# Kernel tuning notes

Measured on AMD Instinct MI355X. Metric: run time of the kernel, lower is better.

Reference implementation:

```python
import jax, jax.numpy as jnp
import numpy as np

B, L, D = 4, 1024, 1024
H = 16
HD = D // H
SCALE = HD ** -0.5
LOCAL_WINDOW = 32
HALF = LOCAL_WINDOW // 2
TEMP = 1.0
PATTERN_TEMP = 1.0
THRESHOLD = 0.1
SPARSITY_RATIO = 0.3
# k for learned sparse topk (eval mode, static given L)
EFF = min(SPARSITY_RATIO, 1.0 - 10.0 / L)
K_TOP = max(1, min(L, int(L * (1.0 - EFF))))


def setup_inputs() -> dict:
    key = jax.random.key(0)
    ks = jax.random.split(key, 16)
    def xavier(k, shape, gain=1.0):
        fan_in, fan_out = shape[1], shape[0]
        a = gain * np.sqrt(6.0 / (fan_in + fan_out))
        return jax.random.uniform(k, shape, jnp.float32, -a, a)
    return {
        'x': jax.random.normal(ks[0], (B, L, D), jnp.float32),
        'w_qkv': xavier(ks[1], (3 * D, D), gain=1.0 / np.sqrt(2.0)),
        'w_proj': xavier(ks[2], (D, D)),
        'b_proj': jnp.zeros((D,), jnp.float32),
        'ps_w1': xavier(ks[3], (D, D), gain=0.5),
        'ps_b1': jnp.zeros((D,), jnp.float32),
        'ln_g': jnp.ones((D,), jnp.float32),
        'ln_b': jnp.zeros((D,), jnp.float32),
        'ps_w2': xavier(ks[4], (D // 2, D), gain=0.5),
        'ps_b2': jnp.zeros((D // 2,), jnp.float32),
        'ps_w3': xavier(ks[5], (3, D // 2), gain=0.5),
        'ps_b3': jnp.zeros((3,), jnp.float32),
        'pattern_bias': jnp.array([0.05, 0.0, -0.05], jnp.float32),
        'sparse_w': jax.random.normal(ks[6], (H, 1, 1), jnp.float32) * 0.1 + 1.0,
        'sparse_b': jnp.zeros((H, 1, 1), jnp.float32),
    }


def _forward(x, w_qkv, w_proj, b_proj, ps_w1, ps_b1, ln_g, ln_b,
             ps_w2, ps_b2, ps_w3, ps_b3, pattern_bias, sparse_w, sparse_b):
    qkv = (x @ w_qkv.T).reshape(B, L, 3, H, HD)
    qkv = jnp.transpose(qkv, (2, 0, 3, 1, 4))  # [3,B,H,L,HD]
    q, k, v = qkv[0], qkv[1], qkv[2]
    scores = jnp.einsum('bhid,bhjd->bhij', q, k) * SCALE  # [B,H,L,L]

    # pattern selector on pooled features
    pooled = (jnp.mean(x, axis=1) + jnp.max(x, axis=1)) / 2.0  # [B,D]
    h = pooled @ ps_w1.T + ps_b1
    mu = jnp.mean(h, axis=-1, keepdims=True)
    var = jnp.mean((h - mu) ** 2, axis=-1, keepdims=True)
    h = (h - mu) / jnp.sqrt(var + 1e-5) * ln_g + ln_b
    h = jax.nn.gelu(h, approximate=False)
    h = jax.nn.gelu(h @ ps_w2.T + ps_b2, approximate=False)
    logits = h @ ps_w3.T + ps_b3 + pattern_bias  # [B,3]
    pw = jax.nn.softmax(logits / PATTERN_TEMP, axis=-1)  # [B,3]

    # learned sparse mask via per-head affine + topk scatter
    s2 = scores * jnp.abs(sparse_w)[None] + sparse_b[None]  # [B,H,L,L]
    _, topk_idx = jax.lax.top_k(s2, K_TOP)  # [B,H,L,K]
    bi = jnp.arange(B)[:, None, None, None]
    hi = jnp.arange(H)[None, :, None, None]
    li = jnp.arange(L)[None, None, :, None]
    sparse_mask = jnp.zeros_like(scores).at[bi, hi, li, topk_idx].set(1.0)

    # local sliding-window mask |i-j| <= HALF
    i = jnp.arange(L)
    local = (jnp.abs(i[:, None] - i[None, :]) <= HALF).astype(jnp.float32)  # [L,L]

    combined = (pw[:, 0, None, None, None] * local[None, None]
                + pw[:, 1, None, None, None]
                + pw[:, 2, None, None, None] * sparse_mask)
    binary = combined > THRESHOLD
    scores = jnp.where(binary, scores, -jnp.inf)

    # fallback: rows fully masked attend only to themselves (score 0)
    all_masked = ~jnp.any(binary, axis=-1)  # [B,H,L]
    eye = jnp.eye(L, dtype=bool)
    scores = jnp.where(all_masked[..., None] & eye[None, None], 0.0, scores)

    attn = jax.nn.softmax(scores / TEMP, axis=-1)
    out = jnp.einsum('bhij,bhjd->bhid', attn, v)  # [B,H,L,HD]
    out = jnp.transpose(out, (0, 2, 1, 3)).reshape(B, L, D)
    return out @ w_proj.T + b_proj


def reference(x, w_qkv, w_proj, b_proj, ps_w1, ps_b1, ln_g, ln_b,
              ps_w2, ps_b2, ps_w3, ps_b3, pattern_bias, sparse_w, sparse_b):
    return _forward(x, w_qkv, w_proj, b_proj, ps_w1, ps_b1, ln_g, ln_b,
                    ps_w2, ps_b2, ps_w3, ps_b3, pattern_bias, sparse_w, sparse_b)
```

## Files before the change

kernel.cpp:

```cpp
#include <hip/hip_runtime.h>
#include <math.h>

#define KTOP_ 716
#define SCALE_ 0.125f
#define QSCALE_ 0.1803368801111731f
#define LN2_ 0.6931471805599453f

typedef float f4v __attribute__((ext_vector_type(4)));
typedef short s8v __attribute__((ext_vector_type(8)));
typedef __bf16 bf8v __attribute__((ext_vector_type(8)));

static __device__ inline unsigned short f2bf(float f) {
  unsigned u = __float_as_uint(f);
  u += 0x7fffu + ((u >> 16) & 1u);
  return (unsigned short)(u >> 16);
}
static __device__ inline unsigned short f2bfn(float f) {
  union { __bf16 b; unsigned short u; } cv;
  cv.b = (__bf16)f;
  return cv.u;
}
static __device__ inline float bf2f(unsigned short h) {
  return __uint_as_float((unsigned)h << 16);
}
static __device__ inline f4v mfma16(s8v a, s8v b, f4v c) {
  union { s8v s; bf8v b; } ua, ub;
  ua.s = a; ub.s = b;
  return __builtin_amdgcn_mfma_f32_16x16x32_bf16(ua.b, ub.b, c, 0, 0, 0);
}
static __device__ inline void gload16(const unsigned short* g, unsigned short* lbase) {
  __builtin_amdgcn_global_load_lds(
      (const __attribute__((address_space(1))) unsigned int*)g,
      (__attribute__((address_space(3))) unsigned int*)lbase, 16, 0, 0);
}

__global__ __launch_bounds__(256) void pool1(const float* __restrict__ x,
                                             float* __restrict__ psum,
                                             float* __restrict__ pmax,
                                             unsigned short* __restrict__ xs) {
  int bid = blockIdx.x;
  int b = bid >> 6, sl = bid & 63;
  int t = threadIdx.x;
  float s[4] = {0.f, 0.f, 0.f, 0.f};
  float m[4] = {-INFINITY, -INFINITY, -INFINITY, -INFINITY};
  const float* xb = x + ((size_t)b << 20) + (size_t)sl * 16 * 1024;
  unsigned short* xo = xs + ((size_t)(b * 1024 + sl * 16)) * 1024;
  for (int l = 0; l < 16; ++l) {
    #pragma unroll
    for (int dg = 0; dg < 4; ++dg) {
      float v = xb[l * 1024 + dg * 256 + t];
      s[dg] += v;
      m[dg] = fmaxf(m[dg], v);
      xo[(size_t)l * 1024 + dg * 256 + t] = f2bfn(v);
    }
  }
  #pragma unroll
  for (int dg = 0; dg < 4; ++dg) {
    psum[(size_t)bid * 1024 + dg * 256 + t] = s[dg];
    pmax[(size_t)bid * 1024 + dg * 256 + t] = m[dg];
  }
}

__global__ __launch_bounds__(256) void ps_gemv1(const float* __restrict__ psum,
                                                const float* __restrict__ pmax,
                                                const float* __restrict__ w1,
                                                const float* __restrict__ b1,
                                                float* __restrict__ h1) {
  __shared__ float pool_s[1024];
  int bid = blockIdx.x;
  int b = bid >> 4, og = bid & 15;
  int t = threadIdx.x;
  #pragma unroll
  for (int i = 0; i < 4; ++i) {
    int d = t + 256 * i;
    float s = 0.f, m = -INFINITY;
    #pragma unroll 8
    for (int sl = 0; sl < 64; ++sl) {
      s += psum[((size_t)b * 64 + sl) * 1024 + d];
      m = fmaxf(m, pmax[((size_t)b * 64 + sl) * 1024 + d]);
    }
    pool_s[d] = (s * (1.0f / 1024.0f) + m) * 0.5f;
  }
  __syncthreads();
  int ol = t >> 2, ks = t & 3;
  int o = og * 64 + ol;
  const float4* wr = (const float4*)(w1 + (size_t)o * 1024 + ks * 256);
  const float4* pp = (const float4*)(&pool_s[ks * 256]);
  float acc = 0.f;
  #pragma unroll 8
  for (int j = 0; j < 64; ++j) {
    float4 a = wr[j], p = pp[j];
    acc += a.x * p.x + a.y * p.y + a.z * p.z + a.w * p.w;
  }
  acc += __shfl_xor(acc, 1, 64);
  acc += __shfl_xor(acc, 2, 64);
  if (ks == 0) h1[b * 1024 + o] = acc + b1[o];
}

__global__ __launch_bounds__(256) void ps_gemv2(const float* __restrict__ h1,
                                                const float* __restrict__ lng,
                                                const float* __restrict__ lnb,
                                                const float* __restrict__ w2,
                                                const float* __restrict__ b2,
                                                float* __restrict__ h2) {
  __shared__ float hs[1024];
  __shared__ float red[256];
  int bid = blockIdx.x;
  int b = bid >> 3, og = bid & 7;
  int t = threadIdx.x;
  const float* hb = h1 + b * 1024;
  float v0[4];
  float ls = 0.f;
  #pragma unroll
  for (int i = 0; i < 4; ++i) { v0[i] = hb[t + 256 * i]; ls += v0[i]; }
  red[t] = ls; __syncthreads();
  for (int s = 128; s > 0; s >>= 1) { if (t < s) red[t] += red[t + s]; __syncthreads(); }
  float mean = red[0] * (1.0f / 1024.0f);
  __syncthreads();
  float lq = 0.f;
  #pragma unroll
  for (int i = 0; i < 4; ++i) { float dv = v0[i] - mean; lq += dv * dv; }
  red[t] = lq; __syncthreads();
  for (int s = 128; s > 0; s >>= 1) { if (t < s) red[t] += red[t + s]; __syncthreads(); }
  float rstd = 1.0f / sqrtf(red[0] * (1.0f / 1024.0f) + 1e-5f);
  #pragma unroll
  for (int i = 0; i < 4; ++i) {
    float v = (v0[i] - mean) * rstd * lng[t + 256 * i] + lnb[t + 256 * i];
    hs[t + 256 * i] = 0.5f * v * (1.0f + erff(v * 0.70710678118654752f));
  }
  __syncthreads();
  int ol = t >> 2, ks = t & 3;
  int o = og * 64 + ol;
  const float4* wr = (const float4*)(w2 + (size_t)o * 1024 + ks * 256);
  const float4* pp = (const float4*)(&hs[ks * 256]);
  float acc = 0.f;
  #pragma unroll 8
  for (int j = 0; j < 64; ++j) {
    float4 a = wr[j], p = pp[j];
    acc += a.x * p.x + a.y * p.y + a.z * p.z + a.w * p.w;
  }
  acc += __shfl_xor(acc, 1, 64);
  acc += __shfl_xor(acc, 2, 64);
  if (ks == 0) {
    float v = acc + b2[o];
    h2[b * 512 + o] = 0.5f * v * (1.0f + erff(v * 0.70710678118654752f));
  }
}

__global__ __launch_bounds__(256) void ps_logits(const float* __restrict__ h2,
                                                 const float* __restrict__ w3,
                                                 const float* __restrict__ b3,
                                                 const float* __restrict__ pb,
                                                 int* __restrict__ meta) {
  __shared__ float red[256];
  int b = blockIdx.x, t = threadIdx.x;
  float lgv[3];
  for (int c = 0; c < 3; ++c) {
    float p = 0.f;
    for (int i = t; i < 512; i += 256) p += h2[b * 512 + i] * w3[c * 512 + i];
    red[t] = p; __syncthreads();
    for (int s = 128; s > 0; s >>= 1) { if (t < s) red[t] += red[t + s]; __syncthreads(); }
    lgv[c] = red[0] + b3[c] + pb[c];
    __syncthreads();
  }
  if (t == 0) {
    float mx = fmaxf(lgv[0], fmaxf(lgv[1], lgv[2]));
    float e0 = __expf(lgv[0] - mx), e1 = __expf(lgv[1] - mx), e2 = __expf(lgv[2] - mx);
    float inv = 1.0f / (e0 + e1 + e2);
    float p0 = e0 * inv, p1 = e1 * inv, p2 = e2 * inv;
    float c00 = p1;
    float c10 = p0 + p1;
    float c01 = p1 + p2;
    float c11 = (p0 + p1) + p2;
    int t00 = c00 > 0.1f, t10 = c10 > 0.1f, t01 = c01 > 0.1f, t11 = c11 > 0.1f;
    meta[b * 8 + 0] = t00;
    meta[b * 8 + 1] = t10;
    meta[b * 8 + 2] = t01;
    meta[b * 8 + 3] = t11;
    meta[b * 8 + 4] = (t00 != t01) || (t10 != t11);
  }
}

__global__ __launch_bounds__(256) void prep_w(const float* __restrict__ w_qkv,
                                              const float* __restrict__ w_proj,
                                              unsigned short* __restrict__ wqs,
                                              unsigned short* __restrict__ wps) {
  int i = blockIdx.x * 256 + threadIdx.x;
  const float* src;
  unsigned short* dst;
  int idx;
  if (i < 786432) { src = w_qkv; dst = wqs; idx = i; }
  else            { src = w_proj; dst = wps; idx = i - 786432; }
  float4 v = ((const float4*)src)[idx];
  ushort4 o;
  o.x = f2bfn(v.x); o.y = f2bfn(v.y); o.z = f2bfn(v.z); o.w = f2bfn(v.w);
  *(ushort4*)(dst + (size_t)idx * 4) = o;
}

template <int MODE, int TM>
__global__ __launch_bounds__(256) void gemm_sp(
    const unsigned short* __restrict__ A, const unsigned short* __restrict__ B,
    const float* __restrict__ bias,
    unsigned short* __restrict__ qxo, unsigned short* __restrict__ kxo,
    unsigned short* __restrict__ vxo,
    float* __restrict__ out, int Nb) {
  constexpr int MFR = TM / 32;
  __shared__ unsigned short Asm[2][TM * 64];
  __shared__ unsigned short Bsm[2][128 * 64];

  int bid = blockIdx.x;
  int bm, bn;
  if (MODE == 0) {
    int xcd = bid & 7, idx = bid >> 3;
    int rb = (xcd >> 1) * 8, cb = (xcd & 1) * 12;
    int r, c;
    if (idx < 64) { r = idx & 7; c = idx >> 3; }
    else          { int j = idx - 64; r = j & 7; c = 8 + (j >> 3); }
    bm = rb + r; bn = cb + c;
  } else {
    int cpx = gridDim.x >> 3;
    int g = (bid & 7) * cpx + (bid >> 3);
    bm = g / Nb; bn = g % Nb;
  }
  size_t row0 = (size_t)bm * TM, col0 = (size_t)bn * 128;

  int tid = threadIdx.x, lane = tid & 63, wv = tid >> 6;
  int wm = (wv >> 1) * (MFR * 16), wn = (wv & 1) << 6;
  int rowg = lane >> 4, colc = lane & 15;

  f4v acc[MFR][4];
  #pragma unroll
  for (int mf = 0; mf < MFR; ++mf)
    #pragma unroll
    for (int nf = 0; nf < 4; ++nf) acc[mf][nf] = (f4v){0.f, 0.f, 0.f, 0.f};

  const unsigned short* Abase = A + row0 * 1024;
  const unsigned short* Bbase = B + col0 * 1024;

  auto STAGE = [&](int kb, int buf) {
    #pragma unroll
    for (int p = 0; p < TM / 32; ++p) {
      int idx = p * 256 + tid;
      int row = idx >> 3;
      int sc = (idx & 7) ^ (row & 7);
      gload16(Abase + (size_t)row * 1024 + kb + sc * 8,
              &Asm[buf][(size_t)(p * 256 + wv * 64) * 8]);
    }
    #pragma unroll
    for (int p = 0; p < 4; ++p) {
      int idx = p * 256 + tid;
      int row = idx >> 3;
      int sc = (idx & 7) ^ (row & 7);
      gload16(Bbase + (size_t)row * 1024 + kb + sc * 8,
              &Bsm[buf][(size_t)(p * 256 + wv * 64) * 8]);
    }
  };

  STAGE(0, 0);
  __syncthreads();
  int cur = 0;

  for (int kb = 0; kb < 1024; kb += 64) {
    if (kb + 64 < 1024) STAGE(kb + 64, cur ^ 1);
    #pragma unroll
    for (int ks = 0; ks < 2; ++ks) {
      s8v af[MFR], bf_[4];
      #pragma unroll
      for (int mf = 0; mf < MFR; ++mf) {
        int row = wm + mf * 16 + colc;
        int kby = (ks * 64 + rowg * 16) ^ ((row & 7) << 4);
        af[mf] = *(const s8v*)((const char*)&Asm[cur][0] + row * 128 + kby);
      }
      #pragma unroll
      for (int nf = 0; nf < 4; ++nf) {
        int row = wn + nf * 16 + colc;
        int kby = (ks * 64 + rowg * 16) ^ ((row & 7) << 4);
        bf_[nf] = *(const s8v*)((const char*)&Bsm[cur][0] + row * 128 + kby);
      }
      #pragma unroll
      for (int mf = 0; mf < MFR; ++mf)
        #pragma unroll
        for (int nf = 0; nf < 4; ++nf)
          acc[mf][nf] = mfma16(af[mf], bf_[nf], acc[mf][nf]);
    }
    __syncthreads();
    cur ^= 1;
  }

  if (MODE == 0) {
    int c = (int)(col0 >> 10);
    #pragma unroll
    for (int mf = 0; mf < MFR; ++mf) {
      int m0 = (int)row0 + wm + mf * 16 + rowg * 4;
      int bb = m0 >> 10, l0 = m0 & 1023;
      #pragma unroll
      for (int nf = 0; nf < 4; ++nf) {
        int n = (int)col0 + wn + nf * 16 + colc;
        int hh = (n >> 6) & 15, hd = n & 63;
        int bhl = bb * 16 + hh;
        if (c == 2) {
          ushort4 h4;
          h4.x = f2bfn(acc[mf][nf][0]);
          h4.y = f2bfn(acc[mf][nf][1]);
          h4.z = f2bfn(acc[mf][nf][2]);
          h4.w = f2bfn(acc[mf][nf][3]);
          *(ushort4*)(vxo + ((size_t)bhl * 64 + hd) * 1024 + l0) = h4;
        } else {
          unsigned short* dst = ((c == 0) ? qxo : kxo) +
                                ((size_t)bhl * 1024 + l0) * 64 + hd;
          float sc_ = (c == 0) ? QSCALE_ : 1.0f;
          #pragma unroll
          for (int r = 0; r < 4; ++r)
            dst[(size_t)r * 64] = f2bfn(acc[mf][nf][r] * sc_);
        }
      }
    }
  } else {
    #pragma unroll
    for (int mf = 0; mf < MFR; ++mf) {
      #pragma unroll
      for (int r = 0; r < 4; ++r) {
        int m = (int)row0 + wm + mf * 16 + rowg * 4 + r;
        #pragma unroll
        for (int nf = 0; nf < 4; ++nf) {
          int n = (int)col0 + wn + nf * 16 + colc;
          out[(size_t)m * 1024 + n] = acc[mf][nf][r] + bias[n];
        }
      }
    }
  }
}

__global__ __launch_bounds__(256) void attn_flash(
    const unsigned short* __restrict__ qx, const unsigned short* __restrict__ kx,
    const unsigned short* __restrict__ vx, const int* __restrict__ meta,
    unsigned short* __restrict__ ao) {
  int n = blockIdx.x;
  int bh = ((n & 7) << 3) | (n >> 7);
  int qt = (n >> 3) & 15;
  int b = bh >> 4, h = bh & 15;
  const int* mb = meta + b * 8;
  if (mb[4]) return;
  int t00 = mb[0], t10 = mb[1];

  int tid = threadIdx.x, lane = tid & 63, wv = tid >> 6;
  int g = lane >> 4, colc = lane & 15;
  int q0 = qt * 64 + wv * 16;

  if (!t10) {
    #pragma unroll
    for (int it = 0; it < 4; ++it) {
      int idx = tid + it * 256;
      int r = idx >> 4, dc = (idx & 15) * 4;
      ushort4 o;
      unsigned short* op = (unsigned short*)&o;
      #pragma unroll
      for (int j = 0; j < 4; ++j)
        op[j] = vx[((size_t)bh * 64 + dc + j) * 1024 + qt * 64 + r];
      *(ushort4*)(ao + ((size_t)b * 1024 + qt * 64 + r) * 1024 + h * 64 + dc) = o;
    }
    return;
  }
  bool local_only = !t00;

  __shared__ __align__(16) unsigned short Ksm[2][64 * 64];
  __shared__ __align__(16) unsigned short Vsm[2][64 * 64];
  __shared__ __align__(16) unsigned short px[4][16][64];

  const unsigned short* qb = qx + ((size_t)bh * 1024 + q0 + colc) * 64 + g * 8;
  s8v Q0 = *(const s8v*)(qb);
  s8v Q1 = *(const s8v*)(qb + 32);

  f4v O[4];
  #pragma unroll
  for (int df = 0; df < 4; ++df) O[df] = (f4v){0.f, 0.f, 0.f, 0.f};
  float m = -1e30f, lsum = 0.f;

  const unsigned short* kxb = kx + ((size_t)bh << 10) * 64;
  const unsigned short* vxb = vx + ((size_t)bh << 16);
  int bq0 = qt * 64;

  int jb_lo = 0, jb_hi = 15;
  if (local_only) {
    int lo = (bq0 - 16) >> 6, hi = (bq0 + 79) >> 6;
    jb_lo = lo < 0 ? 0 : lo;
    jb_hi = hi > 15 ? 15 : hi;
  }

  auto STAGE = [&](int jb2, int buf) {
    int jc = jb2 << 6;
    #pragma unroll
    for (int p = 0; p < 2; ++p) {
      int cidx = p * 256 + tid;
      int row = cidx >> 3;
      int sc = (cidx & 7) ^ (row & 7);
      gload16(kxb + (size_t)(jc + row) * 64 + sc * 8,
              &Ksm[buf][(size_t)(p * 256 + wv * 64) * 8]);
      gload16(vxb + (size_t)row * 1024 + jc + sc * 8,
              &Vsm[buf][(size_t)(p * 256 + wv * 64) * 8]);
    }
  };

  STAGE(jb_lo, 0);
  __syncthreads();
  int cur = 0;
  int swk = (colc & 7) << 4;
  int sx = (colc & 7) << 1;

  for (int jb = jb_lo; jb <= jb_hi; ++jb) {
    if (jb < jb_hi) STAGE(jb + 1, cur ^ 1);

    int jc0 = jb << 6;
    bool wact = !(local_only && (jc0 + 63 < q0 - 16 || jc0 > q0 + 31));
    if (wact) {
      f4v s[4];
      #pragma unroll
      for (int jf = 0; jf < 4; ++jf) {
        const char* kp = (const char*)&Ksm[cur][0] + (jf * 16 + colc) * 128;
        s8v K0 = *(const s8v*)(kp + ((g * 16) ^ swk));
        s8v K1 = *(const s8v*)(kp + ((64 + g * 16) ^ swk));
        f4v acc = (f4v){0.f, 0.f, 0.f, 0.f};
        acc = mfma16(K0, Q0, acc);
        acc = mfma16(K1, Q1, acc);
        s[jf] = acc;
      }

      if (local_only) {
        int i = q0 + colc;
        #pragma unroll
        for (int jf = 0; jf < 4; ++jf)
          #pragma unroll
          for (int r = 0; r < 4; ++r) {
            int j = jc0 + jf * 16 + 4 * g + r;
            int dj = i - j;
            if (dj > 16 || dj < -16) s[jf][r] = -1e30f;
          }
      }

      float cm = fmaxf(
          fmaxf(fmaxf(fmaxf(s[0][0], s[0][1]), fmaxf(s[0][2], s[0][3])),
                fmaxf(fmaxf(s[1][0], s[1][1]), fmaxf(s[1][2], s[1][3]))),
          fmaxf(fmaxf(fmaxf(s[2][0], s[2][1]), fmaxf(s[2][2], s[2][3])),
                fmaxf(fmaxf(s[3][0], s[3][1]), fmaxf(s[3][2], s[3][3]))));
      cm = fmaxf(cm, __shfl_xor(cm, 16, 64));
      cm = fmaxf(cm, __shfl_xor(cm, 32, 64));

      if (__any(cm > m + 8.0f)) {
        float mn = fmaxf(m, cm);
        float fac = __builtin_amdgcn_exp2f(m - mn);
        m = mn;
        lsum *= fac;
        float fo[4];
        #pragma unroll
        for (int r = 0; r < 4; ++r)
          fo[r] = __shfl(fac, (lane & 48) + g * 4 + r, 64);
        #pragma unroll
        for (int df = 0; df < 4; ++df)
          #pragma unroll
          for (int r = 0; r < 4; ++r) O[df][r] *= fo[r];
      }

      float psum = 0.f;
      #pragma unroll
      for (int jf = 0; jf < 4; ++jf) {
        float p0 = __builtin_amdgcn_exp2f(s[jf][0] - m);
        float p1 = __builtin_amdgcn_exp2f(s[jf][1] - m);
        float p2 = __builtin_amdgcn_exp2f(s[jf][2] - m);
        float p3 = __builtin_amdgcn_exp2f(s[jf][3] - m);
        psum += (p0 + p1) + (p2 + p3);
        ushort4 pk;
        pk.x = f2bfn(p0); pk.y = f2bfn(p1); pk.z = f2bfn(p2); pk.w = f2bfn(p3);
        *(ushort4*)&px[wv][colc][4 * ((jf * 4 + g) ^ sx)] = pk;
      }
      psum += __shfl_xor(psum, 16, 64);
      psum += __shfl_xor(psum, 32, 64);
      lsum += psum;

      s8v Pf[2];
      #pragma unroll
      for (int ks = 0; ks < 2; ++ks)
        Pf[ks] = *(const s8v*)&px[wv][colc][4 * ((ks * 8 + 2 * g) ^ sx)];
      #pragma unroll
      for (int df = 0; df < 4; ++df) {
        const char* vp = (const char*)&Vsm[cur][0] + (df * 16 + colc) * 128;
        #pragma unroll
        for (int ks = 0; ks < 2; ++ks) {
          s8v Vf = *(const s8v*)(vp + ((ks * 64 + g * 16) ^ swk));
          O[df] = mfma16(Pf[ks], Vf, O[df]);
        }
      }
    }
    __syncthreads();
    cur ^= 1;
  }

  float linv[4];
  #pragma unroll
  for (int r = 0; r < 4; ++r)
    linv[r] = 1.0f / __shfl(lsum, (lane & 48) + g * 4 + r, 64);
  #pragma unroll
  for (int df = 0; df < 4; ++df) {
    #pragma unroll
    for (int r = 0; r < 4; ++r) {
      int i = q0 + g * 4 + r;
      ao[((size_t)b * 1024 + i) * 1024 + h * 64 + df * 16 + colc] =
          f2bfn(O[df][r] * linv[r]);
    }
  }
}

__global__ __launch_bounds__(256) void attn_sparse(
    const unsigned short* __restrict__ qx, const unsigned short* __restrict__ kx,
    const unsigned short* __restrict__ vx, const int* __restrict__ meta,
    unsigned short* __restrict__ ao) {
  __shared__ float S[32][1028];
  __shared__ float qs[32][68];
  __shared__ float kc[64][68];
  __shared__ float rowsum_s[32];

  int tid = threadIdx.x;
  int lane = tid & 63;
  int wv = tid >> 6;
  int id = blockIdx.x;
  int rt = id & 31;
  int h = (id >> 5) & 15;
  int b = id >> 9;
  int bh = b * 16 + h;
  int row0 = rt * 32;

  const int* mb = meta + b * 8;
  int t00 = mb[0], t10 = mb[1], t01 = mb[2], t11 = mb[3], needs = mb[4];
  if (!needs) return;

  #pragma unroll
  for (int i = 0; i < 8; ++i) {
    int idx = tid + 256 * i;
    int r = idx >> 6, d = idx & 63;
    qs[r][d] = bf2f(qx[((size_t)bh * 1024 + row0 + r) * 64 + d]);
  }

  int lr = lane >> 4, lc = lane & 15;
  int r_a = wv * 8 + lr * 2;
  int r_b = r_a + 1;

  for (int cb = 0; cb < 16; ++cb) {
    __syncthreads();
    #pragma unroll
    for (int i = 0; i < 2; ++i) {
      int idx = tid + 256 * i;
      int cc = idx >> 3, d0 = (idx & 7) * 8;
      union { s8v v; unsigned short u[8]; } kv8;
      kv8.v = *(const s8v*)(kx + ((size_t)bh * 1024 + cb * 64 + cc) * 64 + d0);
      #pragma unroll
      for (int j = 0; j < 8; ++j) kc[cc][d0 + j] = bf2f(kv8.u[j]);
    }
    __syncthreads();

    float acc0[4] = {0.f, 0.f, 0.f, 0.f};
    float acc1[4] = {0.f, 0.f, 0.f, 0.f};
    for (int dq = 0; dq < 64; dq += 4) {
      float4 qa = *(const float4*)&qs[r_a][dq];
      float4 qb = *(const float4*)&qs[r_b][dq];
      #pragma unroll
      for (int cj = 0; cj < 4; ++cj) {
        float4 kv = *(const float4*)&kc[lc + 16 * cj][dq];
        acc0[cj] += qa.x * kv.x + qa.y * kv.y + qa.z * kv.z + qa.w * kv.w;
        acc1[cj] += qb.x * kv.x + qb.y * kv.y + qb.z * kv.z + qb.w * kv.w;
      }
    }
    #pragma unroll
    for (int cj = 0; cj < 4; ++cj) {
      S[r_a][cb * 64 + lc + 16 * cj] = acc0[cj] * LN2_;
      S[r_b][cb * 64 + lc + 16 * cj] = acc1[cj] * LN2_;
    }
  }

  for (int rr = 0; rr < 8; ++rr) {
    int r = wv * 8 + rr;
    int grow = row0 + r;
    float sv[16];
    unsigned kv[16];
    #pragma unroll
    for (int i2 = 0; i2 < 16; ++i2) {
      float s = S[r][lane + 64 * i2];
      sv[i2] = s;
      unsigned u = __float_as_uint(s);
      kv[i2] = (u & 0x80000000u) ? ~u : (u | 0x80000000u);
    }
    unsigned T = 0u;
    for (int bit = 31; bit >= 0; --bit) {
      unsigned cand = T | (1u << bit);
      int cnt = 0;
      #pragma unroll
      for (int i2 = 0; i2 < 16; ++i2) cnt += (kv[i2] >= cand) ? 1 : 0;
      for (int off = 32; off; off >>= 1) cnt += __shfl_xor(cnt, off, 64);
      if (cnt >= KTOP_) T = cand;
    }
    float mx = -INFINITY;
    int kept = 0;
    unsigned kmask = 0;
    #pragma unroll
    for (int i2 = 0; i2 < 16; ++i2) {
      int j = lane + 64 * i2;
      int sp = (kv[i2] >= T) ? 1 : 0;
      int dj = grow - j;
      int lo = (dj <= 16 && dj >= -16) ? 1 : 0;
      int keep = sp ? (lo ? t11 : t01) : (lo ? t10 : t00);
      kept += keep;
      if (keep) { kmask |= (1u << i2); mx = fmaxf(mx, sv[i2]); }
    }
    for (int off = 32; off; off >>= 1) {
      mx = fmaxf(mx, __shfl_xor(mx, off, 64));
      kept += __shfl_xor(kept, off, 64);
    }
    if (kept == 0) {
      #pragma unroll
      for (int i2 = 0; i2 < 16; ++i2) {
        int j = lane + 64 * i2;
        S[r][j] = (j == grow) ? 1.0f : 0.0f;
      }
      if (lane == 0) rowsum_s[r] = 1.0f;
    } else {
      float sum = 0.f;
      #pragma unroll
      for (int i2 = 0; i2 < 16; ++i2) {
        float p = ((kmask >> i2) & 1u) ? __expf(sv[i2] - mx) : 0.0f;
        sum += p;
        S[r][lane + 64 * i2] = p;
      }
      for (int off = 32; off; off >>= 1) sum += __shfl_xor(sum, off, 64);
      if (lane == 0) rowsum_s[r] = sum;
    }
  }

  int ld = lane & 15;
  int d0 = ld * 4;
  float4 oa0 = make_float4(0.f, 0.f, 0.f, 0.f);
  float4 oa1 = make_float4(0.f, 0.f, 0.f, 0.f);
  for (int vb = 0; vb < 16; ++vb) {
    __syncthreads();
    #pragma unroll
    for (int i = 0; i < 2; ++i) {
      int idx = tid + 256 * i;
      int d = idx >> 3, c0 = (idx & 7) * 8;
      union { s8v v; unsigned short u[8]; } vv8;
      vv8.v = *(const s8v*)(vx + ((size_t)bh * 64 + d) * 1024 + vb * 64 + c0);
      #pragma unroll
      for (int j = 0; j < 8; ++j) kc[c0 + j][d] = bf2f(vv8.u[j]);
    }
    __syncthreads();
    for (int cq = 0; cq < 64; cq += 4) {
      float4 pa = *(const float4*)&S[r_a][vb * 64 + cq];
      float4 pb = *(const float4*)&S[r_b][vb * 64 + cq];
      float par[4] = {pa.x, pa.y, pa.z, pa.w};
      float pbr[4] = {pb.x, pb.y, pb.z, pb.w};
      #pragma unroll
      for (int tt = 0; tt < 4; ++tt) {
        float4 vv = *(const float4*)&kc[cq + tt][d0];
        oa0.x += par[tt] * vv.x; oa0.y += par[tt] * vv.y;
        oa0.z += par[tt] * vv.z; oa0.w += par[tt] * vv.w;
        oa1.x += pbr[tt] * vv.x; oa1.y += pbr[tt] * vv.y;
        oa1.z += pbr[tt] * vv.z; oa1.w += pbr[tt] * vv.w;
      }
    }
  }
  float inv0 = 1.0f / rowsum_s[r_a];
  float inv1 = 1.0f / rowsum_s[r_b];
  ushort4 o0, o1;
  unsigned short* o0p = (unsigned short*)&o0;
  unsigned short* o1p = (unsigned short*)&o1;
  float v0[4] = {oa0.x * inv0, oa0.y * inv0, oa0.z * inv0, oa0.w * inv0};
  float v1[4] = {oa1.x * inv1, oa1.y * inv1, oa1.z * inv1, oa1.w * inv1};
  #pragma unroll
  for (int j = 0; j < 4; ++j) {
    o0p[j] = f2bf(v0[j]);
    o1p[j] = f2bf(v1[j]);
  }
  *(ushort4*)(ao + ((size_t)b * 1024 + row0 + r_a) * 1024 + h * 64 + d0) = o0;
  *(ushort4*)(ao + ((size_t)b * 1024 + row0 + r_b) * 1024 + h * 64 + d0) = o1;
}

__global__ __launch_bounds__(256) void pool_kernel(const float* __restrict__ x,
                                                   float* __restrict__ pooled) {
  int g = blockIdx.x * 256 + threadIdx.x;
  int b = g >> 10, d = g & 1023;
  const float* xp = x + ((size_t)b << 20) + d;
  float s = 0.f, m = -INFINITY;
  #pragma unroll 4
  for (int l = 0; l < 1024; ++l) {
    float v = xp[(size_t)l << 10];
    s += v;
    m = fmaxf(m, v);
  }
  pooled[g] = (s * (1.0f / 1024.0f) + m) * 0.5f;
}

__global__ __launch_bounds__(256) void qkv_gemm(const float* __restrict__ X,
                                                const float* __restrict__ W,
                                                float* __restrict__ qw,
                                                float* __restrict__ kw,
                                                float* __restrict__ vw) {
  __shared__ float As[8][128];
  __shared__ float Bs[8][128];
  int tid = threadIdx.x;
  int row0 = blockIdx.y * 128, col0 = blockIdx.x * 128;
  int lr = tid >> 1;
  int lk = (tid & 1) * 4;
  int ty = tid >> 4, tx = tid & 15;
  float acc[8][8] = {};

  for (int kb = 0; kb < 1024; kb += 8) {
    float4 a4 = *(const float4*)(X + (size_t)(row0 + lr) * 1024 + kb + lk);
    float4 b4 = *(const float4*)(W + (size_t)(col0 + lr) * 1024 + kb + lk);
    __syncthreads();
    As[lk + 0][lr] = a4.x; As[lk + 1][lr] = a4.y; As[lk + 2][lr] = a4.z; As[lk + 3][lr] = a4.w;
    Bs[lk + 0][lr] = b4.x; Bs[lk + 1][lr] = b4.y; Bs[lk + 2][lr] = b4.z; Bs[lk + 3][lr] = b4.w;
    __syncthreads();
    #pragma unroll
    for (int kk = 0; kk < 8; ++kk) {
      float av[8], bv[8];
      #pragma unroll
      for (int i = 0; i < 8; ++i) av[i] = As[kk][ty * 8 + i];
      #pragma unroll
      for (int j = 0; j < 8; ++j) bv[j] = Bs[kk][tx * 8 + j];
      #pragma unroll
      for (int i = 0; i < 8; ++i)
        #pragma unroll
        for (int j = 0; j < 8; ++j) acc[i][j] += av[i] * bv[j];
    }
  }
  #pragma unroll
  for (int i = 0; i < 8; ++i) {
    int m = row0 + ty * 8 + i;
    int bb = m >> 10, l = m & 1023;
    #pragma unroll
    for (int j = 0; j < 8; j += 4) {
      int n = col0 + tx * 8 + j;
      int c = n >> 10;
      int hh = (n >> 6) & 15;
      int hd = n & 63;
      float* base = (c == 0) ? qw : (c == 1) ? kw : vw;
      float* dst = base + ((size_t)(bb * 16 + hh) * 1024 + l) * 64 + hd;
      *(float4*)dst = make_float4(acc[i][j], acc[i][j + 1], acc[i][j + 2], acc[i][j + 3]);
    }
  }
}

__global__ __launch_bounds__(256) void proj_gemm(const float* __restrict__ A,
                                                 const float* __restrict__ W,
                                                 const float* __restrict__ bias,
                                                 float* __restrict__ out) {
  __shared__ float As[8][128];
  __shared__ float Bs[8][128];
  int tid = threadIdx.x;
  int row0 = blockIdx.y * 128, col0 = blockIdx.x * 128;
  int lr = tid >> 1;
  int lk = (tid & 1) * 4;
  int ty = tid >> 4, tx = tid & 15;
  float acc[8][8] = {};

  for (int kb = 0; kb < 1024; kb += 8) {
    float4 a4 = *(const float4*)(A + (size_t)(row0 + lr) * 1024 + kb + lk);
    float4 b4 = *(const float4*)(W + (size_t)(col0 + lr) * 1024 + kb + lk);
    __syncthreads();
    As[lk + 0][lr] = a4.x; As[lk + 1][lr] = a4.y; As[lk + 2][lr] = a4.z; As[lk + 3][lr] = a4.w;
    Bs[lk + 0][lr] = b4.x; Bs[lk + 1][lr] = b4.y; Bs[lk + 2][lr] = b4.z; Bs[lk + 3][lr] = b4.w;
    __syncthreads();
    #pragma unroll
    for (int kk = 0; kk < 8; ++kk) {
      float av[8], bv[8];
      #pragma unroll
      for (int i = 0; i < 8; ++i) av[i] = As[kk][ty * 8 + i];
      #pragma unroll
      for (int j = 0; j < 8; ++j) bv[j] = Bs[kk][tx * 8 + j];
      #pragma unroll
      for (int i = 0; i < 8; ++i)
        #pragma unroll
        for (int j = 0; j < 8; ++j) acc[i][j] += av[i] * bv[j];
    }
  }
  #pragma unroll
  for (int i = 0; i < 8; ++i) {
    int m = row0 + ty * 8 + i;
    #pragma unroll
    for (int j = 0; j < 8; j += 4) {
      int n = col0 + tx * 8 + j;
      *(float4*)(out + (size_t)m * 1024 + n) =
          make_float4(acc[i][j] + bias[n], acc[i][j + 1] + bias[n + 1],
                      acc[i][j + 2] + bias[n + 2], acc[i][j + 3] + bias[n + 3]);
    }
  }
}

__global__ __launch_bounds__(256) void pattern_kernel(
    const float* __restrict__ pooled,
    const float* __restrict__ w1, const float* __restrict__ b1,
    const float* __restrict__ lng, const float* __restrict__ lnb,
    const float* __restrict__ w2, const float* __restrict__ b2,
    const float* __restrict__ w3, const float* __restrict__ b3,
    const float* __restrict__ pb, int* __restrict__ meta) {
  __shared__ float pool_s[1024];
  __shared__ float h1[1024];
  __shared__ float h2[512];
  __shared__ float red[256];
  int b = blockIdx.x, t = threadIdx.x;

  for (int i = t; i < 1024; i += 256) pool_s[i] = pooled[b * 1024 + i];
  __syncthreads();
  for (int o = t; o < 1024; o += 256) {
    float acc = b1[o];
    const float* wr = w1 + (size_t)o * 1024;
    for (int k = 0; k < 1024; ++k) acc += pool_s[k] * wr[k];
    h1[o] = acc;
  }
  __syncthreads();
  float ls = 0.f;
  for (int i = t; i < 1024; i += 256) ls += h1[i];
  red[t] = ls; __syncthreads();
  for (int s = 128; s > 0; s >>= 1) { if (t < s) red[t] += red[t + s]; __syncthreads(); }
  float mean = red[0] * (1.0f / 1024.0f);
  __syncthreads();
  float lq = 0.f;
  for (int i = t; i < 1024; i += 256) { float dv = h1[i] - mean; lq += dv * dv; }
  red[t] = lq; __syncthreads();
  for (int s = 128; s > 0; s >>= 1) { if (t < s) red[t] += red[t + s]; __syncthreads(); }
  float var = red[0] * (1.0f / 1024.0f);
  float rstd = 1.0f / sqrtf(var + 1e-5f);
  __syncthreads();
  for (int i = t; i < 1024; i += 256) {
    float v = (h1[i] - mean) * rstd * lng[i] + lnb[i];
    h1[i] = 0.5f * v * (1.0f + erff(v * 0.70710678118654752f));
  }
  __syncthreads();
  for (int o = t; o < 512; o += 256) {
    float acc = b2[o];
    const float* wr = w2 + (size_t)o * 1024;
    for (int k = 0; k < 1024; ++k) acc += h1[k] * wr[k];
    h2[o] = 0.5f * acc * (1.0f + erff(acc * 0.70710678118654752f));
  }
  __syncthreads();
  float lgv[3];
  for (int c = 0; c < 3; ++c) {
    float p = 0.f;
    for (int i = t; i < 512; i += 256) p += h2[i] * w3[c * 512 + i];
    __syncthreads();
    red[t] = p; __syncthreads();
    for (int s = 128; s > 0; s >>= 1) { if (t < s) red[t] += red[t + s]; __syncthreads(); }
    lgv[c] = red[0] + b3[c] + pb[c];
  }
  if (t == 0) {
    float mx = fmaxf(lgv[0], fmaxf(lgv[1], lgv[2]));
    float e0 = __expf(lgv[0] - mx), e1 = __expf(lgv[1] - mx), e2 = __expf(lgv[2] - mx);
    float inv = 1.0f / (e0 + e1 + e2);
    float p0 = e0 * inv, p1 = e1 * inv, p2 = e2 * inv;
    float c00 = p1;
    float c10 = p0 + p1;
    float c01 = p1 + p2;
    float c11 = (p0 + p1) + p2;
    int t00 = c00 > 0.1f, t10 = c10 > 0.1f, t01 = c01 > 0.1f, t11 = c11 > 0.1f;
    meta[b * 8 + 0] = t00;
    meta[b * 8 + 1] = t10;
    meta[b * 8 + 2] = t01;
    meta[b * 8 + 3] = t11;
    meta[b * 8 + 4] = (t00 != t01) || (t10 != t11);
  }
}

__global__ __launch_bounds__(256) void attn_kernel_f32(const float* __restrict__ qw,
                                                       const float* __restrict__ kw,
                                                       const float* __restrict__ vw,
                                                       const int* __restrict__ meta,
                                                       float* __restrict__ ao) {
  __shared__ float S[32][1028];
  __shared__ float qs[32][68];
  __shared__ float kc[64][68];
  __shared__ float rowsum_s[32];

  int tid = threadIdx.x;
  int lane = tid & 63;
  int wv = tid >> 6;
  int id = blockIdx.x;
  int rt = id & 31;
  int h = (id >> 5) & 15;
  int b = id >> 9;
  int bh = b * 16 + h;
  int row0 = rt * 32;

  const int* mb = meta + b * 8;
  int t00 = mb[0], t10 = mb[1], t01 = mb[2], t11 = mb[3], needs = mb[4];

  {
    const float4* qp = (const float4*)(qw + ((size_t)bh * 1024 + row0 + wv * 8) * 64);
    #pragma unroll
    for (int i = 0; i < 2; ++i) {
      int f = lane + 64 * i;
      float4 v = qp[f];
      int r = wv * 8 + (f >> 4);
      int d = (f & 15) << 2;
      qs[r][d] = v.x; qs[r][d + 1] = v.y; qs[r][d + 2] = v.z; qs[r][d + 3] = v.w;
    }
  }

  int lr = lane >> 4, lc = lane & 15;
  int r_a = wv * 8 + lr * 2;
  int r_b = r_a + 1;

  for (int cb = 0; cb < 16; ++cb) {
    __syncthreads();
    const float4* kp = (const float4*)(kw + ((size_t)bh * 1024 + cb * 64) * 64);
    #pragma unroll
    for (int i = 0; i < 4; ++i) {
      int f = tid + 256 * i;
      float4 v = kp[f];
      int c = f >> 4, d = (f & 15) << 2;
      kc[c][d] = v.x; kc[c][d + 1] = v.y; kc[c][d + 2] = v.z; kc[c][d + 3] = v.w;
    }
    __syncthreads();

    float acc0[4] = {0.f, 0.f, 0.f, 0.f};
    float acc1[4] = {0.f, 0.f, 0.f, 0.f};
    for (int dq = 0; dq < 64; dq += 4) {
      float4 qa = *(const float4*)&qs[r_a][dq];
      float4 qb = *(const float4*)&qs[r_b][dq];
      #pragma unroll
      for (int cj = 0; cj < 4; ++cj) {
        float4 kv = *(const float4*)&kc[lc + 16 * cj][dq];
        acc0[cj] += qa.x * kv.x + qa.y * kv.y + qa.z * kv.z + qa.w * kv.w;
        acc1[cj] += qb.x * kv.x + qb.y * kv.y + qb.z * kv.z + qb.w * kv.w;
      }
    }
    #pragma unroll
    for (int cj = 0; cj < 4; ++cj) {
      S[r_a][cb * 64 + lc + 16 * cj] = acc0[cj] * SCALE_;
      S[r_b][cb * 64 + lc + 16 * cj] = acc1[cj] * SCALE_;
    }
  }

  for (int rr = 0; rr < 8; ++rr) {
    int r = wv * 8 + rr;
    int grow = row0 + r;
    float sv[16];
    unsigned kv[16];
    #pragma unroll
    for (int i2 = 0; i2 < 16; ++i2) {
      float s = S[r][lane + 64 * i2];
      sv[i2] = s;
      unsigned u = __float_as_uint(s);
      kv[i2] = (u & 0x80000000u) ? ~u : (u | 0x80000000u);
    }
    unsigned T = 0u;
    if (needs) {
      for (int bit = 31; bit >= 0; --bit) {
        unsigned cand = T | (1u << bit);
        int cnt = 0;
        #pragma unroll
        for (int i2 = 0; i2 < 16; ++i2) cnt += (kv[i2] >= cand) ? 1 : 0;
        for (int off = 32; off; off >>= 1) cnt += __shfl_xor(cnt, off, 64);
        if (cnt >= KTOP_) T = cand;
      }
    }
    float mx = -INFINITY;
    int kept = 0;
    unsigned kmask = 0;
    #pragma unroll
    for (int i2 = 0; i2 < 16; ++i2) {
      int j = lane + 64 * i2;
      int sp = (kv[i2] >= T) ? 1 : 0;
      int dj = grow - j;
      int lo = (dj <= 16 && dj >= -16) ? 1 : 0;
      int keep = sp ? (lo ? t11 : t01) : (lo ? t10 : t00);
      kept += keep;
      if (keep) { kmask |= (1u << i2); mx = fmaxf(mx, sv[i2]); }
    }
    for (int off = 32; off; off >>= 1) {
      mx = fmaxf(mx, __shfl_xor(mx, off, 64));
      kept += __shfl_xor(kept, off, 64);
    }
    if (kept == 0) {
      #pragma unroll
      for (int i2 = 0; i2 < 16; ++i2) {
        int j = lane + 64 * i2;
        S[r][j] = (j == grow) ? 1.0f : 0.0f;
      }
      if (lane == 0) rowsum_s[r] = 1.0f;
    } else {
      float sum = 0.f;
      #pragma unroll
      for (int i2 = 0; i2 < 16; ++i2) {
        float p = ((kmask >> i2) & 1u) ? __expf(sv[i2] - mx) : 0.0f;
        sum += p;
        S[r][lane + 64 * i2] = p;
      }
      for (int off = 32; off; off >>= 1) sum += __shfl_xor(sum, off, 64);
      if (lane == 0) rowsum_s[r] = sum;
    }
  }

  int ld = lane & 15;
  int d0 = ld * 4;
  float4 oa0 = make_float4(0.f, 0.f, 0.f, 0.f);
  float4 oa1 = make_float4(0.f, 0.f, 0.f, 0.f);
  for (int vb = 0; vb < 16; ++vb) {
    __syncthreads();
    const float4* vp = (const float4*)(vw + ((size_t)bh * 1024 + vb * 64) * 64);
    #pragma unroll
    for (int i = 0; i < 4; ++i) {
      int f = tid + 256 * i;
      float4 v = vp[f];
      int c = f >> 4, d = (f & 15) << 2;
      kc[c][d] = v.x; kc[c][d + 1] = v.y; kc[c][d + 2] = v.z; kc[c][d + 3] = v.w;
    }
    __syncthreads();
    for (int cq = 0; cq < 64; cq += 4) {
      float4 pa = *(const float4*)&S[r_a][vb * 64 + cq];
      float4 pb = *(const float4*)&S[r_b][vb * 64 + cq];
      float par[4] = {pa.x, pa.y, pa.z, pa.w};
      float pbr[4] = {pb.x, pb.y, pb.z, pb.w};
      #pragma unroll
      for (int tt = 0; tt < 4; ++tt) {
        float4 vv = *(const float4*)&kc[cq + tt][d0];
        oa0.x += par[tt] * vv.x; oa0.y += par[tt] * vv.y;
        oa0.z += par[tt] * vv.z; oa0.w += par[tt] * vv.w;
        oa1.x += pbr[tt] * vv.x; oa1.y += pbr[tt] * vv.y;
        oa1.z += pbr[tt] * vv.z; oa1.w += pbr[tt] * vv.w;
      }
    }
  }
  float inv0 = 1.0f / rowsum_s[r_a];
  float inv1 = 1.0f / rowsum_s[r_b];
  float* p0 = ao + ((size_t)b * 1024 + row0 + r_a) * 1024 + h * 64 + d0;
  float* p1 = ao + ((size_t)b * 1024 + row0 + r_b) * 1024 + h * 64 + d0;
  *(float4*)p0 = make_float4(oa0.x * inv0, oa0.y * inv0, oa0.z * inv0, oa0.w * inv0);
  *(float4*)p1 = make_float4(oa1.x * inv1, oa1.y * inv1, oa1.z * inv1, oa1.w * inv1);
}

extern "C" void kernel_launch(void* const* d_in, const int* in_sizes, int n_in,
                              void* d_out, int out_size, void* d_ws, size_t ws_size,
                              hipStream_t stream) {
  const float* x      = (const float*)d_in[0];
  const float* w_qkv  = (const float*)d_in[1];
  const float* w_proj = (const float*)d_in[2];
  const float* b_proj = (const float*)d_in[3];
  const float* ps_w1  = (const float*)d_in[4];
  const float* ps_b1  = (const float*)d_in[5];
  const float* ln_g   = (const float*)d_in[6];
  const float* ln_b   = (const float*)d_in[7];
  const float* ps_w2  = (const float*)d_in[8];
  const float* ps_b2  = (const float*)d_in[9];
  const float* ps_w3  = (const float*)d_in[10];
  const float* ps_b3  = (const float*)d_in[11];
  const float* pbias  = (const float*)d_in[12];

  float* ws = (float*)d_ws;
  float* pooled = ws;
  int*   meta   = (int*)(ws + 4096);
  float* h1buf  = ws + 8192;
  float* h2buf  = ws + 12288;
  float* ppsum  = ws + 16384;
  float* ppmax  = ws + 278528;
  float* qw = ws + 1048576;
  float* kw = qw + 4194304;
  float* vw = kw + 4194304;
  float* ao = vw + 4194304;
  unsigned short* u16b = (unsigned short*)(ao + 4194304);
  unsigned short* xs   = u16b;
  unsigned short* wqs  = xs + 4194304;
  unsigned short* wps  = wqs + 3145728;
  unsigned short* aos  = wps + 1048576;
  unsigned short* qx   = aos + 4194304;
  unsigned short* kx   = qx + 4194304;
  unsigned short* vx   = kx + 4194304;
  float* out = (float*)d_out;

  const size_t NEED_FULL = (size_t)(1048576 + 4 * 4194304) * 4 +
                           (size_t)(4194304 + 3145728 + 1048576 + 4194304 +
                                    3 * 4194304) * 2;

  if (ws_size >= NEED_FULL) {
    pool1<<<256, 256, 0, stream>>>(x, ppsum, ppmax, xs);
    ps_gemv1<<<64, 256, 0, stream>>>(ppsum, ppmax, ps_w1, ps_b1, h1buf);
    ps_gemv2<<<32, 256, 0, stream>>>(h1buf, ln_g, ln_b, ps_w2, ps_b2, h2buf);
    ps_logits<<<4, 256, 0, stream>>>(h2buf, ps_w3, ps_b3, pbias, meta);

    prep_w<<<4096, 256, 0, stream>>>(w_qkv, w_proj, wqs, wps);
    gemm_sp<0, 128><<<768, 256, 0, stream>>>(xs, wqs, nullptr, qx, kx, vx,
                                             nullptr, 24);

    attn_flash<<<1024, 256, 0, stream>>>(qx, kx, vx, meta, aos);
    attn_sparse<<<2048, 256, 0, stream>>>(qx, kx, vx, meta, aos);

    gemm_sp<1, 64><<<512, 256, 0, stream>>>(aos, wps, b_proj,
                                            nullptr, nullptr, nullptr, out, 8);
  } else {
    pool_kernel<<<16, 256, 0, stream>>>(x, pooled);
    pattern_kernel<<<4, 256, 0, stream>>>(pooled, ps_w1, ps_b1, ln_g, ln_b,
                                          ps_w2, ps_b2, ps_w3, ps_b3, pbias, meta);
    qkv_gemm<<<dim3(24, 32), 256, 0, stream>>>(x, w_qkv, qw, kw, vw);
    attn_kernel_f32<<<2048, 256, 0, stream>>>(qw, kw, vw, meta, ao);
    proj_gemm<<<dim3(8, 32), 256, 0, stream>>>(ao, w_proj, b_proj, out);
  }
}
```

Before: 147.8 us.

## Double query tile per block in flash attention with unrolled ping-pong buffers

The flash attention kernel now runs 512 threads per block, each covering 128 query rows instead of 64, so each staged K/V tile is reused by eight waves and half as many blocks reload K/V. The double-buffer loop is manually unrolled into two named shared buffers, which removes the dynamic buffer index. MFMA sections are wrapped in s_setprio hints. The costs are fewer blocks in flight, wider windows for local-only tiles (so more waves sit idle during those iterations), and a block-wide barrier across more waves.

New measurement: 140.1 us. 1.06x faster.

```diff
diff --git a/kernel.cpp b/kernel.cpp
--- a/kernel.cpp
+++ b/kernel.cpp
@@ -331,13 +331,13 @@
   }
 }
 
-__global__ __launch_bounds__(256) void attn_flash(
+__global__ __launch_bounds__(512) void attn_flash(
     const unsigned short* __restrict__ qx, const unsigned short* __restrict__ kx,
     const unsigned short* __restrict__ vx, const int* __restrict__ meta,
     unsigned short* __restrict__ ao) {
   int n = blockIdx.x;
-  int bh = ((n & 7) << 3) | (n >> 7);
-  int qt = (n >> 3) & 15;
+  int bh = ((n & 7) << 3) | (n >> 6);
+  int qt2 = (n >> 3) & 7;
   int b = bh >> 4, h = bh & 15;
   const int* mb = meta + b * 8;
   if (mb[4]) return;
@@ -345,27 +345,30 @@
 
   int tid = threadIdx.x, lane = tid & 63, wv = tid >> 6;
   int g = lane >> 4, colc = lane & 15;
-  int q0 = qt * 64 + wv * 16;
+  int bq0 = qt2 * 128;
+  int q0 = bq0 + wv * 16;
 
   if (!t10) {
     #pragma unroll
     for (int it = 0; it < 4; ++it) {
-      int idx = tid + it * 256;
+      int idx = tid + it * 512;
       int r = idx >> 4, dc = (idx & 15) * 4;
       ushort4 o;
       unsigned short* op = (unsigned short*)&o;
       #pragma unroll
       for (int j = 0; j < 4; ++j)
-        op[j] = vx[((size_t)bh * 64 + dc + j) * 1024 + qt * 64 + r];
-      *(ushort4*)(ao + ((size_t)b * 1024 + qt * 64 + r) * 1024 + h * 64 + dc) = o;
+        op[j] = vx[((size_t)bh * 64 + dc + j) * 1024 + bq0 + r];
+      *(ushort4*)(ao + ((size_t)b * 1024 + bq0 + r) * 1024 + h * 64 + dc) = o;
     }
     return;
   }
   bool local_only = !t00;
 
-  __shared__ __align__(16) unsigned short Ksm[2][64 * 64];
-  __shared__ __align__(16) unsigned short Vsm[2][64 * 64];
-  __shared__ __align__(16) unsigned short px[4][16][64];
+  __shared__ __align__(16) unsigned short KsmA[64 * 64];
+  __shared__ __align__(16) unsigned short KsmB[64 * 64];
+  __shared__ __align__(16) unsigned short VsmA[64 * 64];
+  __shared__ __align__(16) unsigned short VsmB[64 * 64];
+  __shared__ __align__(16) unsigned short px[8][16][64];
 
   const unsigned short* qb = qx + ((size_t)bh * 1024 + q0 + colc) * 64 + g * 8;
   s8v Q0 = *(const s8v*)(qb);
@@ -378,120 +381,125 @@
 
   const unsigned short* kxb = kx + ((size_t)bh << 10) * 64;
   const unsigned short* vxb = vx + ((size_t)bh << 16);
-  int bq0 = qt * 64;
 
   int jb_lo = 0, jb_hi = 15;
   if (local_only) {
-    int lo = (bq0 - 16) >> 6, hi = (bq0 + 79) >> 6;
+    int lo = (bq0 - 16) >> 6, hi = (bq0 + 143) >> 6;
     jb_lo = lo < 0 ? 0 : lo;
     jb_hi = hi > 15 ? 15 : hi;
   }
 
-  auto STAGE = [&](int jb2, int buf) {
+  int srow = tid >> 3;
+  int ssc = (tid & 7) ^ (srow & 7);
+  auto STAGE = [&](int jb2, unsigned short* Kd, unsigned short* Vd) {
     int jc = jb2 << 6;
-    #pragma unroll
-    for (int p = 0; p < 2; ++p) {
-      int cidx = p * 256 + tid;
-      int row = cidx >> 3;
-      int sc = (cidx & 7) ^ (row & 7);
-      gload16(kxb + (size_t)(jc + row) * 64 + sc * 8,
-              &Ksm[buf][(size_t)(p * 256 + wv * 64) * 8]);
-      gload16(vxb + (size_t)row * 1024 + jc + sc * 8,
-              &Vsm[buf][(size_t)(p * 256 + wv * 64) * 8]);
-    }
+    unsigned short* lbase_k = Kd + (size_t)(wv * 64) * 8;
+    unsigned short* lbase_v = Vd + (size_t)(wv * 64) * 8;
+    gload16(kxb + (size_t)(jc + srow) * 64 + ssc * 8, lbase_k);
+    gload16(vxb + (size_t)srow * 1024 + jc + ssc * 8, lbase_v);
   };
 
-  STAGE(jb_lo, 0);
-  __syncthreads();
-  int cur = 0;
   int swk = (colc & 7) << 4;
   int sx = (colc & 7) << 1;
 
-  for (int jb = jb_lo; jb <= jb_hi; ++jb) {
-    if (jb < jb_hi) STAGE(jb + 1, cur ^ 1);
-
-    int jc0 = jb << 6;
-    bool wact = !(local_only && (jc0 + 63 < q0 - 16 || jc0 > q0 + 31));
-    if (wact) {
-      f4v s[4];
-      #pragma unroll
-      for (int jf = 0; jf < 4; ++jf) {
-        const char* kp = (const char*)&Ksm[cur][0] + (jf * 16 + colc) * 128;
-        s8v K0 = *(const s8v*)(kp + ((g * 16) ^ swk));
-        s8v K1 = *(const s8v*)(kp + ((64 + g * 16) ^ swk));
-        f4v acc = (f4v){0.f, 0.f, 0.f, 0.f};
-        acc = mfma16(K0, Q0, acc);
-        acc = mfma16(K1, Q1, acc);
-        s[jf] = acc;
-      }
-
-      if (local_only) {
-        int i = q0 + colc;
+  auto COMPUTE = [&](int jc0, const char* Kb, const char* Vb) {
+    if (local_only && (jc0 + 63 < q0 - 16 || jc0 > q0 + 31)) return;
+    f4v s[4];
+    __builtin_amdgcn_s_setprio(1);
+    #pragma unroll
+    for (int jf = 0; jf < 4; ++jf) {
+      const char* kp = Kb + (jf * 16 + colc) * 128;
+      s8v K0 = *(const s8v*)(kp + ((g * 16) ^ swk));
+      s8v K1 = *(const s8v*)(kp + ((64 + g * 16) ^ swk));
+      f4v acc = (f4v){0.f, 0.f, 0.f, 0.f};
+      acc = mfma16(K0, Q0, acc);
+      acc = mfma16(K1, Q1, acc);
+      s[jf] = acc;
+    }
+    __builtin_amdgcn_s_setprio(0);
+
+    if (local_only) {
+      int i = q0 + colc;
+      #pragma unroll
+      for (int jf = 0; jf < 4; ++jf)
         #pragma unroll
-        for (int jf = 0; jf < 4; ++jf)
-          #pragma unroll
-          for (int r = 0; r < 4; ++r) {
-            int j = jc0 + jf * 16 + 4 * g + r;
-            int dj = i - j;
-            if (dj > 16 || dj < -16) s[jf][r] = -1e30f;
-          }
-      }
-
-      float cm = fmaxf(
-          fmaxf(fmaxf(fmaxf(s[0][0], s[0][1]), fmaxf(s[0][2], s[0][3])),
-                fmaxf(fmaxf(s[1][0], s[1][1]), fmaxf(s[1][2], s[1][3]))),
-          fmaxf(fmaxf(fmaxf(s[2][0], s[2][1]), fmaxf(s[2][2], s[2][3])),
-                fmaxf(fmaxf(s[3][0], s[3][1]), fmaxf(s[3][2], s[3][3]))));
-      cm = fmaxf(cm, __shfl_xor(cm, 16, 64));
-      cm = fmaxf(cm, __shfl_xor(cm, 32, 64));
-
-      if (__any(cm > m + 8.0f)) {
-        float mn = fmaxf(m, cm);
-        float fac = __builtin_amdgcn_exp2f(m - mn);
-        m = mn;
-        lsum *= fac;
-        float fo[4];
+        for (int r = 0; r < 4; ++r) {
+          int j = jc0 + jf * 16 + 4 * g + r;
+          int dj = i - j;
+          if (dj > 16 || dj < -16) s[jf][r] = -1e30f;
+        }
+    }
+
+    float cm = fmaxf(
+        fmaxf(fmaxf(fmaxf(s[0][0], s[0][1]), fmaxf(s[0][2], s[0][3])),
+              fmaxf(fmaxf(s[1][0], s[1][1]), fmaxf(s[1][2], s[1][3]))),
+        fmaxf(fmaxf(fmaxf(s[2][0], s[2][1]), fmaxf(s[2][2], s[2][3])),
+              fmaxf(fmaxf(s[3][0], s[3][1]), fmaxf(s[3][2], s[3][3]))));
+    cm = fmaxf(cm, __shfl_xor(cm, 16, 64));
+    cm = fmaxf(cm, __shfl_xor(cm, 32, 64));
+
+    if (__any(cm > m + 8.0f)) {
+      float mn = fmaxf(m, cm);
+      float fac = __builtin_amdgcn_exp2f(m - mn);
+      m = mn;
+      lsum *= fac;
+      float fo[4];
+      #pragma unroll
+      for (int r = 0; r < 4; ++r)
+        fo[r] = __shfl(fac, (lane & 48) + g * 4 + r, 64);
+      #pragma unroll
+      for (int df = 0; df < 4; ++df)
         #pragma unroll
-        for (int r = 0; r < 4; ++r)
-          fo[r] = __shfl(fac, (lane & 48) + g * 4 + r, 64);
-        #pragma unroll
-        for (int df = 0; df < 4; ++df)
-          #pragma unroll
-          for (int r = 0; r < 4; ++r) O[df][r] *= fo[r];
-      }
-
-      float psum = 0.f;
-      #pragma unroll
-      for (int jf = 0; jf < 4; ++jf) {
-        float p0 = __builtin_amdgcn_exp2f(s[jf][0] - m);
-        float p1 = __builtin_amdgcn_exp2f(s[jf][1] - m);
-        float p2 = __builtin_amdgcn_exp2f(s[jf][2] - m);
-        float p3 = __builtin_amdgcn_exp2f(s[jf][3] - m);
-        psum += (p0 + p1) + (p2 + p3);
-        ushort4 pk;
-        pk.x = f2bfn(p0); pk.y = f2bfn(p1); pk.z = f2bfn(p2); pk.w = f2bfn(p3);
-        *(ushort4*)&px[wv][colc][4 * ((jf * 4 + g) ^ sx)] = pk;
-      }
-      psum += __shfl_xor(psum, 16, 64);
-      psum += __shfl_xor(psum, 32, 64);
-      lsum += psum;
-
-      s8v Pf[2];
-      #pragma unroll
-      for (int ks = 0; ks < 2; ++ks)
-        Pf[ks] = *(const s8v*)&px[wv][colc][4 * ((ks * 8 + 2 * g) ^ sx)];
-      #pragma unroll
-      for (int df = 0; df < 4; ++df) {
-        const char* vp = (const char*)&Vsm[cur][0] + (df * 16 + colc) * 128;
-        #pragma unroll
-        for (int ks = 0; ks < 2; ++ks) {
-          s8v Vf = *(const s8v*)(vp + ((ks * 64 + g * 16) ^ swk));
-          O[df] = mfma16(Pf[ks], Vf, O[df]);
-        }
-      }
-    }
-    __syncthreads();
-    cur ^= 1;
+        for (int r = 0; r < 4; ++r) O[df][r] *= fo[r];
+    }
+
+    float psum = 0.f;
+    #pragma unroll
+    for (int jf = 0; jf < 4; ++jf) {
+      float p0 = __builtin_amdgcn_exp2f(s[jf][0] - m);
+      float p1 = __builtin_amdgcn_exp2f(s[jf][1] - m);
+      float p2 = __builtin_amdgcn_exp2f(s[jf][2] - m);
+      float p3 = __builtin_amdgcn_exp2f(s[jf][3] - m);
+      psum += (p0 + p1) + (p2 + p3);
+      ushort4 pk;
+      pk.x = f2bfn(p0); pk.y = f2bfn(p1); pk.z = f2bfn(p2); pk.w = f2bfn(p3);
+      *(ushort4*)&px[wv][colc][4 * ((jf * 4 + g) ^ sx)] = pk;
+    }
+    psum += __shfl_xor(psum, 16, 64);
+    psum += __shfl_xor(psum, 32, 64);
+    lsum += psum;
+
+    s8v Pf[2];
+    #pragma unroll
+    for (int ks = 0; ks < 2; ++ks)
+      Pf[ks] = *(const s8v*)&px[wv][colc][4 * ((ks * 8 + 2 * g) ^ sx)];
+    __builtin_amdgcn_s_setprio(1);
+    #pragma unroll
+    for (int df = 0; df < 4; ++df) {
+      const char* vp = Vb + (df * 16 + colc) * 128;
+      #pragma unroll
+      for (int ks = 0; ks < 2; ++ks) {
+        s8v Vf = *(const s8v*)(vp + ((ks * 64 + g * 16) ^ swk));
+        O[df] = mfma16(Pf[ks], Vf, O[df]);
+      }
+    }
+    __builtin_amdgcn_s_setprio(0);
+  };
+
+  STAGE(jb_lo, KsmA, VsmA);
+  __syncthreads();
+  int jb = jb_lo;
+  while (true) {
+    if (jb + 1 <= jb_hi) STAGE(jb + 1, KsmB, VsmB);
+    COMPUTE(jb << 6, (const char*)KsmA, (const char*)VsmA);
+    __syncthreads();
+    ++jb;
+    if (jb > jb_hi) break;
+    if (jb + 1 <= jb_hi) STAGE(jb + 1, KsmA, VsmA);
+    COMPUTE(jb << 6, (const char*)KsmB, (const char*)VsmB);
+    __syncthreads();
+    ++jb;
+    if (jb > jb_hi) break;
   }
 
   float linv[4];
@@ -1086,7 +1094,7 @@
     gemm_sp<0, 128><<<768, 256, 0, stream>>>(xs, wqs, nullptr, qx, kx, vx,
                                              nullptr, 24);
 
-    attn_flash<<<1024, 256, 0, stream>>>(qx, kx, vx, meta, aos);
+    attn_flash<<<512, 512, 0, stream>>>(qx, kx, vx, meta, aos);
     attn_sparse<<<2048, 256, 0, stream>>>(qx, kx, vx, meta, aos);
 
     gemm_sp<1, 64><<<512, 256, 0, stream>>>(aos, wps, b_proj,
```
